# Performance work log

Measured on AMD Instinct MI355X. Metric: run time of the kernel, lower is better.

## Reference

```python
import jax, jax.numpy as jnp
from jax import lax
import numpy as np
import math

V, D, N, L, KC, KL, B, S = 32000, 1024, 64, 4, 4, 4, 2, 1024
SCALE = 1.0 / math.sqrt(2 * L)   # base_layer.residual_scale
GAMMA = 0.01                     # lindblad_gamma
COND_TH = 100.0                  # condition_threshold
PHASE = np.complex64(np.exp(1j * 0.1))  # quaternionic escape rotation


def setup_inputs() -> dict:
    key = jax.random.key(0)
    ks = jax.random.split(key, 16)
    g = lambda k, shp, s=0.02: jax.random.normal(k, shp, jnp.float32) * s
    return {
        'token_ids': jax.random.randint(ks[0], (B, S), 0, V, dtype=jnp.int32),
        'emb_r': g(ks[1], (V, D)),
        'emb_i': g(ks[2], (V, D)),
        'W_in': g(ks[3], (L, D, 2 * D)),
        'conv_k': g(ks[4], (L, D, KC), 0.2),
        'A_log': jax.random.normal(ks[5], (L, D, N), jnp.float32) * 0.5,
        'dt_scale': g(ks[6], (L, D), 1.0),
        'dt_bias': jnp.full((L, D), -2.0, jnp.float32),
        'W_B': g(ks[7], (L, N, D)),
        'W_C': g(ks[8], (L, N, D)),
        'D_skip': g(ks[9], (L, D), 0.1),
        'W_out': g(ks[10], (L, D, D)),
        'L_ops': g(ks[11], (L, KL, D), 0.1),
        'norm_w': jnp.ones((D,), jnp.float32),
    }


def _dwconv(x, k):
    # causal depthwise conv; x [B,S,D] real, k [D,KC]
    xt = jnp.transpose(x, (0, 2, 1))  # [B,D,S]
    pad = k.shape[-1] - 1
    y = lax.conv_general_dilated(xt, k[:, None, :], (1,), [(pad, 0)],
                                 feature_group_count=k.shape[0])
    return jnp.transpose(y, (0, 2, 1))


def _csilu(x):
    # complex 'silu': x * sigmoid(|x|)
    return x * jax.nn.sigmoid(jnp.abs(x))


def _layer(x, Wi, ck, Alog, dts, dtb, WB, WC, Dk, Wo, Lops):
    residual = x
    xz = jnp.einsum('bsd,de->bse', x, Wi)          # complex [B,S,2D]
    x1, z = xz[..., :D], xz[..., D:]
    x1 = _dwconv(x1.real, ck) + 1j * _dwconv(x1.imag, ck)
    x1 = _csilu(x1)
    dt = jax.nn.softplus(x1.real * dts + dtb)      # [B,S,D] real
    A = -jnp.exp(Alog)                             # [D,N] real, stable
    Bc = jnp.einsum('bsd,nd->bsn', x1, WB)         # complex [B,S,N]
    Cc = jnp.einsum('bsd,nd->bsn', x1, WC)

    def step(h, inp):
        dt_t, x_t, B_t, C_t = inp                  # [B,D],[B,D],[B,N],[B,N]
        decay = jnp.exp(dt_t[..., None] * A)       # [B,D,N] real
        h = decay * h + (dt_t * x_t)[..., None] * B_t[:, None, :]
        y = jnp.einsum('bdn,bn->bd', h, C_t)
        return h, y

    h0 = jnp.zeros((x.shape[0], D, N), jnp.complex64)
    xs = (jnp.transpose(dt, (1, 0, 2)), jnp.transpose(x1, (1, 0, 2)),
          jnp.transpose(Bc, (1, 0, 2)), jnp.transpose(Cc, (1, 0, 2)))
    _, ys = lax.scan(step, h0, xs)                 # [S,B,D]
    y = jnp.transpose(ys, (1, 0, 2)) + Dk * x1
    y = y * _csilu(z)
    branch = jnp.einsum('bsd,de->bse', y, Wo)      # branch_out = (out-res)/scale

    # Lindblad dissipation: psi -> psi - gamma * sum_k L_k (L_k^H psi)
    proj = jnp.einsum('bsd,kd->bsk', branch, Lops)
    branch = branch - GAMMA * jnp.einsum('bsk,kd->bsd', proj, Lops)

    # H_eff = mean_s |psi_s><psi_s|; quaternionic escape uses its conditioning.
    # Only the diagonal is needed for the (diag-approx) condition number.
    diag = jnp.mean(jnp.abs(branch) ** 2, axis=1)  # [B,D]
    cond = jnp.max(diag, -1) / (jnp.min(diag, -1) + 1e-8)
    phase = jnp.where(cond > COND_TH, PHASE, jnp.complex64(1.0))  # [B]
    branch = branch * phase[:, None, None]

    # hybrid automata: _H_prev is None on first forward -> no jump (faithful)
    return residual + SCALE * branch


def reference(token_ids, emb_r, emb_i, W_in, conv_k, A_log, dt_scale, dt_bias,
              W_B, W_C, D_skip, W_out, L_ops, norm_w):
    psi = emb_r[token_ids] + 1j * emb_i[token_ids]   # [B,S,D] complex64
    for l in range(L):
        psi = _layer(psi, W_in[l], conv_k[l], A_log[l], dt_scale[l],
                     dt_bias[l], W_B[l], W_C[l], D_skip[l], W_out[l], L_ops[l])
    # ComplexRMSNorm
    rms = jnp.sqrt(jnp.mean(jnp.abs(psi) ** 2, -1, keepdims=True) + 1e-8)
    psi = psi / rms * norm_w
    # Born collapse sampler with weight tied to real embedding
    amp_r = jnp.einsum('bsd,vd->bsv', psi.real, emb_r)
    amp_i = jnp.einsum('bsd,vd->bsv', psi.imag, emb_r)
    logits = jnp.log(amp_r ** 2 + amp_i ** 2 + 1e-8)  # [B,S,V] real
    return logits
```

## Files before the change

kernel.cpp:

```cpp
#include <hip/hip_runtime.h>
#include <math.h>

#define BB 2
#define SS 1024
#define DD 1024
#define NN 64
#define LLAYERS 4
#define KCC 4
#define KLL 4
#define VV 32000
#define MM (BB*SS)
#define M2 (2*MM)
#define PS ((size_t)MM*DD)
#define CH 4
#define LC (SS/CH)
#define BDW (BB*DD)

#define SCALE_F 0.35355339059327373f
#define GAMMA_F 0.01f
#define PHASE_COS 0.99500416527802576f
#define PHASE_SIN 0.09983341664682815f

typedef _Float16 f16x8 __attribute__((ext_vector_type(8)));
typedef _Float16 f16x4 __attribute__((ext_vector_type(4)));
typedef float f32x4 __attribute__((ext_vector_type(4)));

__device__ __forceinline__ float softplus_f(float x) {
    return fmaxf(x, 0.f) + log1pf(expf(-fabsf(x)));
}

__device__ __forceinline__ void async16(void* lds_dst, const void* g_src) {
    __builtin_amdgcn_global_load_lds(
        (const __attribute__((address_space(1))) unsigned int*)g_src,
        (__attribute__((address_space(3))) unsigned int*)lds_dst,
        16, 0, 0);
}

__device__ __forceinline__ float rsum64_dpp(float v) {
    int x;
    x = __float_as_int(v);
    v += __int_as_float(__builtin_amdgcn_update_dpp(0, x, 0x111, 0xf, 0xf, true));
    x = __float_as_int(v);
    v += __int_as_float(__builtin_amdgcn_update_dpp(0, x, 0x112, 0xf, 0xf, true));
    x = __float_as_int(v);
    v += __int_as_float(__builtin_amdgcn_update_dpp(0, x, 0x114, 0xf, 0xf, true));
    x = __float_as_int(v);
    v += __int_as_float(__builtin_amdgcn_update_dpp(0, x, 0x118, 0xf, 0xf, true));
    x = __float_as_int(v);
    v += __int_as_float(__builtin_amdgcn_update_dpp(0, x, 0x142, 0xa, 0xf, true));
    x = __float_as_int(v);
    v += __int_as_float(__builtin_amdgcn_update_dpp(0, x, 0x143, 0xc, 0xf, true));
    return v;
}

__global__ __launch_bounds__(256) void k_split_w(const float* __restrict__ W,
        _Float16* __restrict__ Wh, _Float16* __restrict__ Wl, int Ksz, int Nsz) {
    __shared__ float t[32][33];
    int k0 = blockIdx.x * 32, n0 = blockIdx.y * 32;
    size_t base = (size_t)blockIdx.z * Ksz * Nsz;
    int r = threadIdx.x >> 3, c4 = (threadIdx.x & 7) * 4;
    float4 v = *(const float4*)(W + base + (size_t)(k0 + r) * Nsz + n0 + c4);
    t[r][c4 + 0] = v.x; t[r][c4 + 1] = v.y; t[r][c4 + 2] = v.z; t[r][c4 + 3] = v.w;
    __syncthreads();
    f16x4 hi, lo;
    #pragma unroll
    for (int j = 0; j < 4; ++j) {
        float x = t[c4 + j][r];
        _Float16 h = (_Float16)x;
        hi[j] = h; lo[j] = (_Float16)(x - (float)h);
    }
    size_t o = base + (size_t)(n0 + r) * Ksz + k0 + c4;
    *(f16x4*)(Wh + o) = hi;
    *(f16x4*)(Wl + o) = lo;
}

__global__ __launch_bounds__(256) void k_embed(const int* __restrict__ tok,
        const float* __restrict__ er, const float* __restrict__ ei,
        float* __restrict__ Pr, float* __restrict__ Pi,
        _Float16* __restrict__ Ph, _Float16* __restrict__ Pl) {
    int i = blockIdx.x * 256 + threadIdx.x;
    int d4 = (i & (DD/4 - 1)) * 4;
    int m  = i >> 8;
    int t = tok[m];
    float4 r  = *(const float4*)(er + (size_t)t * DD + d4);
    float4 im = *(const float4*)(ei + (size_t)t * DD + d4);
    size_t o = (size_t)m * DD + d4;
    *(float4*)(Pr + o) = r;
    *(float4*)(Pi + o) = im;
    float vr[4] = {r.x, r.y, r.z, r.w}, vi[4] = {im.x, im.y, im.z, im.w};
    f16x4 rh, rl, ih, il;
    #pragma unroll
    for (int j = 0; j < 4; ++j) {
        _Float16 h = (_Float16)vr[j]; rh[j] = h; rl[j] = (_Float16)(vr[j] - (float)h);
        _Float16 g = (_Float16)vi[j]; ih[j] = g; il[j] = (_Float16)(vi[j] - (float)g);
    }
    *(f16x4*)(Ph + o) = rh;      *(f16x4*)(Pl + o) = rl;
    *(f16x4*)(Ph + PS + o) = ih; *(f16x4*)(Pl + PS + o) = il;
}

__global__ __launch_bounds__(256, 2) void k_gemm_f16(
        const _Float16* __restrict__ Ah, const _Float16* __restrict__ Al,
        const _Float16* __restrict__ Bh, const _Float16* __restrict__ Bl,
        float* __restrict__ C, int Nsz) {
    __shared__ __align__(16) unsigned char lds[32768];
    const int lane = threadIdx.x & 63;
    const int wid  = threadIdx.x >> 6;
    const int wm = (wid >> 1) * 64;
    const int wv = (wid & 1) * 64;
    const int n0 = blockIdx.x * 128;
    const int m0 = blockIdx.y * 128;
    const int fr = lane & 15, fq = lane >> 4;

    f32x4 acc[4][4] = {};

    for (int k0 = 0; k0 < 1024; k0 += 32) {
        #pragma unroll
        for (int j = 0; j < 8; ++j) {
            int cid = wid * 8 + j;
            int sel = cid >> 3, c = cid & 7;
            const _Float16* bp = (sel == 0) ? Ah : (sel == 1) ? Al : (sel == 2) ? Bh : Bl;
            int rbase = ((sel < 2) ? m0 : n0) + c * 16 + fr;
            async16(lds + cid * 1024, bp + (size_t)rbase * 1024 + k0 + fq * 8);
        }
        __syncthreads();

        f16x8 ah[4], al[4];
        #pragma unroll
        for (int ms = 0; ms < 4; ++ms) {
            int off = ((wm >> 4) + ms) * 1024 + lane * 16;
            ah[ms] = *(const f16x8*)(lds + off);
            al[ms] = *(const f16x8*)(lds + 8192 + off);
        }
        #pragma unroll
        for (int vs = 0; vs < 4; ++vs) {
            int boff = ((wv >> 4) + vs) * 1024 + lane * 16;
            f16x8 bh = *(const f16x8*)(lds + 16384 + boff);
            f16x8 bl = *(const f16x8*)(lds + 24576 + boff);
            #pragma unroll
            for (int ms = 0; ms < 4; ++ms) {
                acc[ms][vs] = __builtin_amdgcn_mfma_f32_16x16x32_f16(ah[ms], bh, acc[ms][vs], 0, 0, 0);
                acc[ms][vs] = __builtin_amdgcn_mfma_f32_16x16x32_f16(ah[ms], bl, acc[ms][vs], 0, 0, 0);
                acc[ms][vs] = __builtin_amdgcn_mfma_f32_16x16x32_f16(al[ms], bh, acc[ms][vs], 0, 0, 0);
            }
        }
        __syncthreads();
    }

    #pragma unroll
    for (int ms = 0; ms < 4; ++ms) {
        #pragma unroll
        for (int vs = 0; vs < 4; ++vs) {
            #pragma unroll
            for (int r = 0; r < 4; ++r) {
                int row = m0 + wm + ms * 16 + fq * 4 + r;
                int col = n0 + wv + vs * 16 + fr;
                C[(size_t)row * Nsz + col] = acc[ms][vs][r];
            }
        }
    }
}

__global__ __launch_bounds__(256) void k_conv(const float* __restrict__ XZ,
        const float* __restrict__ ck, const float* __restrict__ dts,
        const float* __restrict__ dtb,
        float* __restrict__ Xr, float* __restrict__ Xi, float* __restrict__ DT,
        float* __restrict__ ZUr, float* __restrict__ ZUi) {
    int i = blockIdx.x * 256 + threadIdx.x;
    int d = i & (DD - 1);
    int m = i >> 10;
    int b = m >> 10, s = m & (SS - 1);
    float cr = 0.f, ci = 0.f;
    #pragma unroll
    for (int j = 0; j < KCC; ++j) {
        int sj = s - (KCC - 1) + j;
        if (sj >= 0) {
            int mm = (b << 10) + sj;
            float kw = ck[d * KCC + j];
            cr = fmaf(XZ[(size_t)mm * 2048 + d], kw, cr);
            ci = fmaf(XZ[(size_t)(MM + mm) * 2048 + d], kw, ci);
        }
    }
    float mag = sqrtf(cr*cr + ci*ci);
    float sg = 1.f / (1.f + expf(-mag));
    float xr = cr * sg, xi = ci * sg;
    Xr[i] = xr; Xi[i] = xi;
    DT[i] = softplus_f(fmaf(xr, dts[d], dtb[d]));
    float zr = XZ[(size_t)m * 2048 + DD + d];
    float zi = XZ[(size_t)(MM + m) * 2048 + DD + d];
    float mz = sqrtf(zr*zr + zi*zi);
    float sz = 1.f / (1.f + expf(-mz));
    ZUr[i] = zr * sz; ZUi[i] = zi * sz;
}

__global__ __launch_bounds__(256) void k_bc(const float* __restrict__ X,
        const float* __restrict__ WBp, const float* __restrict__ WCp,
        float* __restrict__ BC2) {
    __shared__ float xs[4][DD];
    __shared__ float red[4 * 256];
    int r0 = blockIdx.x * 4;
    for (int f = threadIdx.x; f < 4 * (DD / 4); f += 256) {
        int r = f / (DD / 4), c = (f % (DD / 4)) * 4;
        *(float4*)(&xs[r][c]) = *(const float4*)(X + (size_t)(r0 + r) * DD + c);
    }
    __syncthreads();
    int out = threadIdx.x & 127;
    int half = threadIdx.x >> 7;
    const float* Wrow = (out < 64) ? (WBp + (size_t)out * DD) : (WCp + (size_t)(out - 64) * DD);
    float acc[4] = {0.f, 0.f, 0.f, 0.f};
    for (int k = half * 512; k < half * 512 + 512; k += 4) {
        float4 w = *(const float4*)(Wrow + k);
        #pragma unroll
        for (int r = 0; r < 4; ++r) {
            float4 x4 = *(float4*)(&xs[r][k]);
            acc[r] = fmaf(x4.x, w.x, fmaf(x4.y, w.y, fmaf(x4.z, w.z, fmaf(x4.w, w.w, acc[r]))));
        }
    }
    #pragma unroll
    for (int r = 0; r < 4; ++r) red[r * 256 + threadIdx.x] = acc[r];
    __syncthreads();
    if (threadIdx.x < 128) {
        int isIm = (r0 >= MM) ? 1 : 0;
        int n = out & 63;
        int comp = ((out >> 6) << 1) | isIm;
        #pragma unroll
        for (int r = 0; r < 4; ++r) {
            float v = red[r * 256 + threadIdx.x] + red[r * 256 + threadIdx.x + 128];
            int m = (r0 + r) & (MM - 1);
            BC2[((size_t)m * 64 + n) * 4 + comp] = v;
        }
    }
}

__global__ __launch_bounds__(256, 8) void k_scan1(const float* __restrict__ X,
        const float* __restrict__ DT, const float4* __restrict__ BC2,
        const float* __restrict__ Alog, float* __restrict__ Y2T,
        float2* __restrict__ HB, float* __restrict__ SDT) {
    int w = (blockIdx.x << 2) + (threadIdx.x >> 6);
    int lane = threadIdx.x & 63;
    int c = w & (CH - 1);
    int bd = w >> 2;
    int b = bd >> 10, d = bd & (DD - 1);
    float Av = -__expf(Alog[(size_t)d * NN + lane]);
    float hr = 0.f, hi = 0.f, sdt = 0.f;
    int s0 = c * LC, s1 = s0 + LC;
    size_t mBase = (size_t)(b << 10);
    size_t md = (mBase + s0) * DD + d;
    float dt_c = DT[md], xr_c = X[md], xi_c = X[PS + md];
    float4 bc_c = BC2[(mBase + s0) * 64 + lane];
    size_t ys = (size_t)bd * SS + s0;
    for (int s = s0; s < s1; ++s) {
        int sn = (s + 1 < s1) ? (s + 1) : s;
        size_t mdn = (mBase + sn) * DD + d;
        float dt_n = DT[mdn], xr_n = X[mdn], xi_n = X[PS + mdn];
        float4 bc_n = BC2[(mBase + sn) * 64 + lane];
        float g = __expf(dt_c * Av);
        float dxr = dt_c * xr_c, dxi = dt_c * xi_c;
        hr = fmaf(g, hr, fmaf(dxr, bc_c.x, -dxi * bc_c.y));
        hi = fmaf(g, hi, fmaf(dxr, bc_c.y,  dxi * bc_c.x));
        sdt += dt_c;
        float yr = rsum64_dpp(hr * bc_c.z - hi * bc_c.w);
        float yi = rsum64_dpp(hr * bc_c.w + hi * bc_c.z);
        if (lane == 63) {
            Y2T[ys]      = yr;
            Y2T[PS + ys] = yi;
        }
        ++ys;
        dt_c = dt_n; xr_c = xr_n; xi_c = xi_n; bc_c = bc_n;
    }
    HB[((size_t)c * BDW + bd) * NN + lane] = make_float2(hr, hi);
    if (lane == 0) SDT[c * BDW + bd] = sdt;
}

__global__ __launch_bounds__(256, 8) void k_scan3(const float* __restrict__ DT,
        const float* __restrict__ BC2, const float* __restrict__ Alog,
        const float2* __restrict__ HB, const float* __restrict__ SDT,
        float* __restrict__ Y2T) {
    int w = (blockIdx.x << 2) + (threadIdx.x >> 6);
    int lane = threadIdx.x & 63;
    int cm1 = w >> 11;
    int bd = w & (BDW - 1);
    int b = bd >> 10, d = bd & (DD - 1);
    float Av = -__expf(Alog[(size_t)d * NN + lane]);
    float2 h0 = HB[(size_t)bd * NN + lane];
    float hr = h0.x, hi = h0.y;
    if (cm1 >= 1) {
        float2 h1 = HB[((size_t)1 * BDW + bd) * NN + lane];
        float P1 = __expf(Av * SDT[1 * BDW + bd]);
        hr = fmaf(P1, hr, h1.x); hi = fmaf(P1, hi, h1.y);
        if (cm1 >= 2) {
            float2 h2 = HB[((size_t)2 * BDW + bd) * NN + lane];
            float P2 = __expf(Av * SDT[2 * BDW + bd]);
            hr = fmaf(P2, hr, h2.x); hi = fmaf(P2, hi, h2.y);
        }
    }
    int s0 = (cm1 + 1) * LC, s1 = s0 + LC;
    size_t mBase = (size_t)(b << 10);
    size_t md = (mBase + s0) * DD + d;
    float dt_c = DT[md];
    float2 cc_c = *(const float2*)(BC2 + ((mBase + s0) * 64 + lane) * 4 + 2);
    size_t ys = (size_t)bd * SS + s0;
    for (int s = s0; s < s1; ++s) {
        int sn = (s + 1 < s1) ? (s + 1) : s;
        size_t mdn = (mBase + sn) * DD + d;
        float dt_n = DT[mdn];
        float2 cc_n = *(const float2*)(BC2 + ((mBase + sn) * 64 + lane) * 4 + 2);
        float g = __expf(dt_c * Av);
        hr *= g; hi *= g;
        float yr = rsum64_dpp(hr * cc_c.x - hi * cc_c.y);
        float yi = rsum64_dpp(hr * cc_c.y + hi * cc_c.x);
        if (lane == 63) {
            Y2T[ys]      += yr;
            Y2T[PS + ys] += yi;
        }
        ++ys;
        dt_c = dt_n; cc_c = cc_n;
    }
}

__global__ __launch_bounds__(256) void k_ymod(const float* __restrict__ Y2T,
        const float* __restrict__ X, const float* __restrict__ ZUr,
        const float* __restrict__ ZUi, const float* __restrict__ Dk,
        _Float16* __restrict__ YOh, _Float16* __restrict__ YOl) {
    __shared__ float tr[64][65];
    __shared__ float ti[64][65];
    int d0 = blockIdx.x * 64, m0 = blockIdx.y * 64;
    int b = m0 >> 10, s0 = m0 & (SS - 1);
    int t = threadIdx.x;
    int rr = t >> 2, c0 = (t & 3) * 4;
    size_t ybase = (size_t)(b * DD + d0 + rr) * SS + s0;
    #pragma unroll
    for (int j = 0; j < 4; ++j) {
        float4 vr = *(const float4*)(Y2T + ybase + c0 + j * 16);
        float4 vi = *(const float4*)(Y2T + PS + ybase + c0 + j * 16);
        int sl = c0 + j * 16;
        tr[sl + 0][rr] = vr.x; tr[sl + 1][rr] = vr.y; tr[sl + 2][rr] = vr.z; tr[sl + 3][rr] = vr.w;
        ti[sl + 0][rr] = vi.x; ti[sl + 1][rr] = vi.y; ti[sl + 2][rr] = vi.z; ti[sl + 3][rr] = vi.w;
    }
    __syncthreads();
    int td = t & 63, tq = t >> 6;
    float dk = Dk[d0 + td];
    #pragma unroll
    for (int k = 0; k < 16; ++k) {
        int tm = tq * 16 + k;
        size_t i = (size_t)(m0 + tm) * DD + d0 + td;
        float yr = tr[tm][td];
        float yi = ti[tm][td];
        yr = fmaf(dk, X[i], yr);
        yi = fmaf(dk, X[PS + i], yi);
        float zr = ZUr[i], zi = ZUi[i];
        float or_ = yr * zr - yi * zi;
        float oi_ = yr * zi + yi * zr;
        _Float16 h0 = (_Float16)or_, h1 = (_Float16)oi_;
        YOh[i] = h0;      YOl[i] = (_Float16)(or_ - (float)h0);
        YOh[PS + i] = h1; YOl[PS + i] = (_Float16)(oi_ - (float)h1);
    }
}

__global__ __launch_bounds__(256) void k_projcorr(float* __restrict__ BR,
        const float* __restrict__ Lop) {
    int row = (blockIdx.x << 2) + (threadIdx.x >> 6);
    int lane = threadIdx.x & 63;
    float* br = BR + (size_t)row * DD;
    float4 v[4], lw[4][4];
    float acc[4] = {0.f, 0.f, 0.f, 0.f};
    #pragma unroll
    for (int j = 0; j < 4; ++j) {
        int col = lane * 4 + j * 256;
        v[j] = *(const float4*)(br + col);
        #pragma unroll
        for (int k = 0; k < 4; ++k) {
            lw[j][k] = *(const float4*)(Lop + (size_t)k * DD + col);
            acc[k] += v[j].x * lw[j][k].x + v[j].y * lw[j][k].y
                    + v[j].z * lw[j][k].z + v[j].w * lw[j][k].w;
        }
    }
    #pragma unroll
    for (int off = 1; off <= 32; off <<= 1) {
        #pragma unroll
        for (int k = 0; k < 4; ++k) acc[k] += __shfl_xor(acc[k], off, 64);
    }
    #pragma unroll
    for (int j = 0; j < 4; ++j) {
        int col = lane * 4 + j * 256;
        float4 o;
        o.x = v[j].x - GAMMA_F * (acc[0]*lw[j][0].x + acc[1]*lw[j][1].x + acc[2]*lw[j][2].x + acc[3]*lw[j][3].x);
        o.y = v[j].y - GAMMA_F * (acc[0]*lw[j][0].y + acc[1]*lw[j][1].y + acc[2]*lw[j][2].y + acc[3]*lw[j][3].y);
        o.z = v[j].z - GAMMA_F * (acc[0]*lw[j][0].z + acc[1]*lw[j][1].z + acc[2]*lw[j][2].z + acc[3]*lw[j][3].z);
        o.w = v[j].w - GAMMA_F * (acc[0]*lw[j][0].w + acc[1]*lw[j][1].w + acc[2]*lw[j][2].w + acc[3]*lw[j][3].w);
        *(float4*)(br + col) = o;
    }
}

__global__ __launch_bounds__(256) void k_diag(const float* __restrict__ BR,
        float* __restrict__ DG) {
    __shared__ float red[4][64];
    int b = blockIdx.y, d0 = blockIdx.x * 64;
    int sg = threadIdx.x >> 6, ld = threadIdx.x & 63;
    float acc = 0.f;
    for (int s = sg; s < SS; s += 4) {
        size_t m = (size_t)(b * SS + s) * DD + d0 + ld;
        float r = BR[m], ii = BR[PS + m];
        acc = fmaf(r, r, fmaf(ii, ii, acc));
    }
    red[sg][ld] = acc;
    __syncthreads();
    if (threadIdx.x < 64) {
        float v = red[0][threadIdx.x] + red[1][threadIdx.x] + red[2][threadIdx.x] + red[3][threadIdx.x];
        DG[b * DD + d0 + threadIdx.x] = v * (1.f / SS);
    }
}

__global__ __launch_bounds__(256) void k_phase(const float* __restrict__ DG,
        float* __restrict__ PH) {
    __shared__ float mx[256], mn[256];
    int b = blockIdx.x;
    float vmax = -1e30f, vmin = 1e30f;
    for (int d = threadIdx.x; d < DD; d += 256) {
        float v = DG[b * DD + d];
        vmax = fmaxf(vmax, v); vmin = fminf(vmin, v);
    }
    mx[threadIdx.x] = vmax; mn[threadIdx.x] = vmin;
    __syncthreads();
    for (int st = 128; st >= 1; st >>= 1) {
        if (threadIdx.x < st) {
            mx[threadIdx.x] = fmaxf(mx[threadIdx.x], mx[threadIdx.x + st]);
            mn[threadIdx.x] = fminf(mn[threadIdx.x], mn[threadIdx.x + st]);
        }
        __syncthreads();
    }
    if (threadIdx.x == 0) {
        float cond = mx[0] / (mn[0] + 1e-8f);
        bool ap = cond > 100.0f;
        PH[b * 2 + 0] = ap ? PHASE_COS : 1.f;
        PH[b * 2 + 1] = ap ? PHASE_SIN : 0.f;
    }
}

__global__ __launch_bounds__(256) void k_resid(float* __restrict__ Pr,
        float* __restrict__ Pi, const float* __restrict__ BR,
        const float* __restrict__ PH,
        _Float16* __restrict__ Ph, _Float16* __restrict__ Pl) {
    int i = blockIdx.x * 256 + threadIdx.x;
    int b = i >> 20;
    float pr = PH[b * 2], pih = PH[b * 2 + 1];
    float brr = BR[i], bri = BR[PS + i];
    float nr = fmaf(SCALE_F, brr * pr - bri * pih, Pr[i]);
    float ni = fmaf(SCALE_F, brr * pih + bri * pr, Pi[i]);
    Pr[i] = nr; Pi[i] = ni;
    _Float16 h0 = (_Float16)nr, h1 = (_Float16)ni;
    Ph[i] = h0;      Pl[i] = (_Float16)(nr - (float)h0);
    Ph[PS + i] = h1; Pl[PS + i] = (_Float16)(ni - (float)h1);
}

__global__ __launch_bounds__(256) void k_rms(const float* __restrict__ Pr,
        const float* __restrict__ Pi, const float* __restrict__ nw,
        _Float16* __restrict__ Sp) {
    __shared__ float red[256];
    int m = blockIdx.x;
    int d = threadIdx.x * 4;
    float4 r  = *(const float4*)(Pr + (size_t)m * DD + d);
    float4 ii = *(const float4*)(Pi + (size_t)m * DD + d);
    float acc = r.x*r.x + r.y*r.y + r.z*r.z + r.w*r.w
              + ii.x*ii.x + ii.y*ii.y + ii.z*ii.z + ii.w*ii.w;
    red[threadIdx.x] = acc;
    __syncthreads();
    for (int st = 128; st >= 1; st >>= 1) {
        if (threadIdx.x < st) red[threadIdx.x] += red[threadIdx.x + st];
        __syncthreads();
    }
    float inv = 1.f / sqrtf(red[0] * (1.f / DD) + 1e-8f);
    float4 w = *(const float4*)(nw + d);
    float qr[4] = {r.x*inv*w.x, r.y*inv*w.y, r.z*inv*w.z, r.w*inv*w.w};
    float qi[4] = {ii.x*inv*w.x, ii.y*inv*w.y, ii.z*inv*w.z, ii.w*inv*w.w};
    f16x4 rh, rl, ih, il;
    #pragma unroll
    for (int j = 0; j < 4; ++j) {
        _Float16 h = (_Float16)qr[j]; rh[j] = h; rl[j] = (_Float16)(qr[j] - (float)h);
        _Float16 g = (_Float16)qi[j]; ih[j] = g; il[j] = (_Float16)(qi[j] - (float)g);
    }
    size_t o = (size_t)m * DD + d;
    *(f16x4*)(Sp + o)          = rh;
    *(f16x4*)(Sp + PS + o)     = rl;
    *(f16x4*)(Sp + 2 * PS + o) = ih;
    *(f16x4*)(Sp + 3 * PS + o) = il;
}

__global__ __launch_bounds__(256) void k_split_e(const float* __restrict__ E,
        _Float16* __restrict__ Eh, _Float16* __restrict__ El) {
    size_t i = (size_t)(blockIdx.x * 256 + threadIdx.x) * 8;
    float4 a = *(const float4*)(E + i);
    float4 b = *(const float4*)(E + i + 4);
    float v[8] = {a.x, a.y, a.z, a.w, b.x, b.y, b.z, b.w};
    f16x8 hi, lo;
    #pragma unroll
    for (int j = 0; j < 8; ++j) {
        _Float16 h = (_Float16)v[j];
        hi[j] = h; lo[j] = (_Float16)(v[j] - (float)h);
    }
    *(f16x8*)(Eh + i) = hi;
    *(f16x8*)(El + i) = lo;
}

__global__ __launch_bounds__(256, 2) void k_logits_mfma(
        const _Float16* __restrict__ Sp,
        const _Float16* __restrict__ Eh, const _Float16* __restrict__ El,
        float* __restrict__ out) {
    __shared__ __align__(16) unsigned char lds[49152];
    const int lane = threadIdx.x & 63;
    const int wid  = threadIdx.x >> 6;
    const int wm = (wid >> 1) * 64;
    const int wv = (wid & 1) * 64;
    const int fr = lane & 15, fq = lane >> 4;
    int x = blockIdx.x & 7;
    int j = blockIdx.x >> 3;
    const int m0 = ((x << 1) | (j & 1)) << 7;
    const int v0 = (j >> 1) << 7;

    f32x4 accR[4][4] = {};
    f32x4 accI[4][4] = {};

    for (int k0 = 0; k0 < DD; k0 += 32) {
        #pragma unroll
        for (int jj = 0; jj < 12; ++jj) {
            int cid = jj * 4 + wid;
            const _Float16* src;
            int ldsoff;
            if (cid < 32) {
                int p = cid >> 3, c = cid & 7;
                src = Sp + (size_t)p * PS + (size_t)(m0 + c * 16 + fr) * DD + k0 + fq * 8;
                ldsoff = p * 8192 + c * 1024;
            } else {
                int r = cid - 32;
                int q = r >> 3, c = r & 7;
                const _Float16* Ep = q ? El : Eh;
                src = Ep + (size_t)(v0 + c * 16 + fr) * DD + k0 + fq * 8;
                ldsoff = 32768 + q * 8192 + c * 1024;
            }
            async16(lds + ldsoff, src);
        }
        __syncthreads();

        f16x8 aRh[4], aRl[4], aIh[4], aIl[4];
        #pragma unroll
        for (int ms = 0; ms < 4; ++ms) {
            int off = ((wm >> 4) + ms) * 1024 + lane * 16;
            aRh[ms] = *(const f16x8*)(lds + off);
            aRl[ms] = *(const f16x8*)(lds + 8192 + off);
            aIh[ms] = *(const f16x8*)(lds + 16384 + off);
            aIl[ms] = *(const f16x8*)(lds + 24576 + off);
        }
        #pragma unroll
        for (int vs = 0; vs < 4; ++vs) {
            int boff = ((wv >> 4) + vs) * 1024 + lane * 16;
            f16x8 bh = *(const f16x8*)(lds + 32768 + boff);
            f16x8 bl = *(const f16x8*)(lds + 40960 + boff);
            #pragma unroll
            for (int ms = 0; ms < 4; ++ms) {
                accR[ms][vs] = __builtin_amdgcn_mfma_f32_16x16x32_f16(aRh[ms], bh, accR[ms][vs], 0, 0, 0);
                accR[ms][vs] = __builtin_amdgcn_mfma_f32_16x16x32_f16(aRh[ms], bl, accR[ms][vs], 0, 0, 0);
                accR[ms][vs] = __builtin_amdgcn_mfma_f32_16x16x32_f16(aRl[ms], bh, accR[ms][vs], 0, 0, 0);
                accI[ms][vs] = __builtin_amdgcn_mfma_f32_16x16x32_f16(aIh[ms], bh, accI[ms][vs], 0, 0, 0);
                accI[ms][vs] = __builtin_amdgcn_mfma_f32_16x16x32_f16(aIh[ms], bl, accI[ms][vs], 0, 0, 0);
                accI[ms][vs] = __builtin_amdgcn_mfma_f32_16x16x32_f16(aIl[ms], bh, accI[ms][vs], 0, 0, 0);
            }
        }
        __syncthreads();
    }

    #pragma unroll
    for (int ms = 0; ms < 4; ++ms) {
        #pragma unroll
        for (int vs = 0; vs < 4; ++vs) {
            #pragma unroll
            for (int r = 0; r < 4; ++r) {
                int row = m0 + wm + ms * 16 + fq * 4 + r;
                int col = v0 + wv + vs * 16 + fr;
                float ar = accR[ms][vs][r], ai = accI[ms][vs][r];
                out[(size_t)row * VV + col] = logf(fmaf(ar, ar, fmaf(ai, ai, 1e-8f)));
            }
        }
    }
}

extern "C" void kernel_launch(void* const* d_in, const int* in_sizes, int n_in,
                              void* d_out, int out_size, void* d_ws, size_t ws_size,
                              hipStream_t stream) {
    const int*   tok  = (const int*)d_in[0];
    const float* er   = (const float*)d_in[1];
    const float* ei   = (const float*)d_in[2];
    const float* Win  = (const float*)d_in[3];
    const float* ck   = (const float*)d_in[4];
    const float* Alog = (const float*)d_in[5];
    const float* dts  = (const float*)d_in[6];
    const float* dtb  = (const float*)d_in[7];
    const float* WB   = (const float*)d_in[8];
    const float* WC   = (const float*)d_in[9];
    const float* Dk   = (const float*)d_in[10];
    const float* Wo   = (const float*)d_in[11];
    const float* Lop  = (const float*)d_in[12];
    const float* nw   = (const float*)d_in[13];
    float* out = (float*)d_out;

    float* W0   = (float*)d_ws;
    float* P    = W0;
    float* XZ   = W0 + 2 * PS;
    float* X    = W0 + 6 * PS;
    float* DTp  = W0 + 8 * PS;
    float* ZU   = W0 + 9 * PS;
    float* Y2T  = W0 + 11 * PS;
    _Float16* YOh = (_Float16*)(W0 + 19 * PS);
    _Float16* YOl = (_Float16*)(W0 + 20 * PS);
    _Float16* Ph  = (_Float16*)(W0 + 21 * PS);
    _Float16* Pl  = (_Float16*)(W0 + 22 * PS);
    float* BR   = XZ;
    float* BC2  = W0 + 23 * PS;
    float* DIAG = BC2 + (size_t)MM * 64 * 4;
    float* PH   = DIAG + BB * DD;
    float2* HB  = (float2*)(PH + 16);
    float* SDT  = (float*)(HB + (size_t)CH * BDW * NN);
    _Float16* Winh = (_Float16*)(W0 + 25 * PS);
    _Float16* Winl = (_Float16*)(W0 + 27 * PS);
    _Float16* Woh  = (_Float16*)(W0 + 29 * PS);
    _Float16* Wol  = (_Float16*)(W0 + 30 * PS);
    _Float16* Sp  = (_Float16*)(W0 + 2 * PS);
    _Float16* Ehp = (_Float16*)(W0 + 4 * PS);
    _Float16* Elp = (_Float16*)(W0 + 13 * PS);

    k_split_w<<<dim3(32, 64, 4), 256, 0, stream>>>(Win, Winh, Winl, 1024, 2048);
    k_split_w<<<dim3(32, 32, 4), 256, 0, stream>>>(Wo, Woh, Wol, 1024, 1024);

    k_embed<<<(int)(PS / 4 / 256), 256, 0, stream>>>(tok, er, ei, P, P + PS, Ph, Pl);

    for (int l = 0; l < LLAYERS; ++l) {
        const float* Lopl = Lop + (size_t)l * KLL * DD;
        const float* Alogl = Alog + (size_t)l * DD * NN;
        const _Float16* Wih = Winh + (size_t)l * 2048 * 1024;
        const _Float16* Wil = Winl + (size_t)l * 2048 * 1024;
        const _Float16* Wohl = Woh + (size_t)l * 1024 * 1024;
        const _Float16* Woll = Wol + (size_t)l * 1024 * 1024;

        k_gemm_f16<<<dim3(2048 / 128, M2 / 128), 256, 0, stream>>>(Ph, Pl, Wih, Wil, XZ, 2048);
        k_conv<<<(int)(MM * (size_t)DD / 256), 256, 0, stream>>>(XZ, ck + (size_t)l * DD * KCC,
                dts + l * DD, dtb + l * DD, X, X + PS, DTp, ZU, ZU + PS);
        k_bc<<<M2 / 4, 256, 0, stream>>>(X, WB + (size_t)l * NN * DD, WC + (size_t)l * NN * DD, BC2);
        k_scan1<<<(BDW * CH) / 4, 256, 0, stream>>>(X, DTp, (const float4*)BC2, Alogl, Y2T, HB, SDT);
        k_scan3<<<(BDW * 3) / 4, 256, 0, stream>>>(DTp, BC2, Alogl, HB, SDT, Y2T);
        k_ymod<<<dim3(DD / 64, MM / 64), 256, 0, stream>>>(Y2T, X, ZU, ZU + PS, Dk + l * DD, YOh, YOl);
        k_gemm_f16<<<dim3(1024 / 128, M2 / 128), 256, 0, stream>>>(YOh, YOl, Wohl, Woll, BR, 1024);
        k_projcorr<<<M2 / 4, 256, 0, stream>>>(BR, Lopl);
        k_diag<<<dim3(DD / 64, BB), 256, 0, stream>>>(BR, DIAG);
        k_phase<<<BB, 256, 0, stream>>>(DIAG, PH);
        k_resid<<<(int)(PS / 256), 256, 0, stream>>>(P, P + PS, BR, PH, Ph, Pl);
    }

    k_rms<<<MM, 256, 0, stream>>>(P, P + PS, nw, Sp);
    k_split_e<<<(int)((size_t)VV * DD / 8 / 256), 256, 0, stream>>>(er, Ehp, Elp);
    k_logits_mfma<<<4000, 256, 0, stream>>>(Sp, Ehp, Elp, out);
}
```

Measured before the change: 3.636 ms.

## Vectorize conv and residual kernels, add N64 GEMM tile, nontemporal logits stores

k_conv and k_resid now process four elements per thread with float4 and f16x4 loads and stores, which cuts instruction count and widens memory transactions. The output-projection GEMM switches to a new 128x64-tile kernel, giving twice as many blocks for N=1024 and better CU occupancy. The logits kernel writes its large output with nontemporal stores to avoid polluting the cache. These are several independent bandwidth and occupancy tweaks, and the main risk is that the new GEMM has lower per-block reuse.

Result: no change. 3.594 ms (-1.2%).

```diff
diff --git a/kernel.cpp b/kernel.cpp
--- a/kernel.cpp
+++ b/kernel.cpp
@@ -160,36 +160,136 @@
     }
 }
 
+__global__ __launch_bounds__(256, 2) void k_gemm_n64(
+        const _Float16* __restrict__ Ah, const _Float16* __restrict__ Al,
+        const _Float16* __restrict__ Bh, const _Float16* __restrict__ Bl,
+        float* __restrict__ C, int Nsz) {
+    __shared__ __align__(16) unsigned char lds[24576];
+    const int lane = threadIdx.x & 63;
+    const int wid  = threadIdx.x >> 6;
+    const int wm = (wid >> 1) * 64;
+    const int wv = (wid & 1) * 32;
+    const int n0 = blockIdx.x * 64;
+    const int m0 = blockIdx.y * 128;
+    const int fr = lane & 15, fq = lane >> 4;
+
+    f32x4 acc[4][2] = {};
+
+    for (int k0 = 0; k0 < 1024; k0 += 32) {
+        #pragma unroll
+        for (int j = 0; j < 6; ++j) {
+            int cid = j * 4 + wid;
+            const _Float16* bp;
+            int rbase, ldsoff;
+            if (cid < 16) {
+                bp = (cid >> 3) ? Al : Ah;
+                rbase = m0 + (cid & 7) * 16 + fr;
+                ldsoff = cid * 1024;
+            } else {
+                int r = cid - 16;
+                bp = (r >> 2) ? Bl : Bh;
+                rbase = n0 + (r & 3) * 16 + fr;
+                ldsoff = 16384 + r * 1024;
+            }
+            async16(lds + ldsoff, bp + (size_t)rbase * 1024 + k0 + fq * 8);
+        }
+        __syncthreads();
+
+        f16x8 ah[4], al[4];
+        #pragma unroll
+        for (int ms = 0; ms < 4; ++ms) {
+            int off = ((wm >> 4) + ms) * 1024 + lane * 16;
+            ah[ms] = *(const f16x8*)(lds + off);
+            al[ms] = *(const f16x8*)(lds + 8192 + off);
+        }
+        #pragma unroll
+        for (int vs = 0; vs < 2; ++vs) {
+            int boff = ((wv >> 4) + vs) * 1024 + lane * 16;
+            f16x8 bh = *(const f16x8*)(lds + 16384 + boff);
+            f16x8 bl = *(const f16x8*)(lds + 20480 + boff);
+            #pragma unroll
+            for (int ms = 0; ms < 4; ++ms) {
+                acc[ms][vs] = __builtin_amdgcn_mfma_f32_16x16x32_f16(ah[ms], bh, acc[ms][vs], 0, 0, 0);
+                acc[ms][vs] = __builtin_amdgcn_mfma_f32_16x16x32_f16(ah[ms], bl, acc[ms][vs], 0, 0, 0);
+                acc[ms][vs] = __builtin_amdgcn_mfma_f32_16x16x32_f16(al[ms], bh, acc[ms][vs], 0, 0, 0);
+            }
+        }
+        __syncthreads();
+    }
+
+    #pragma unroll
+    for (int ms = 0; ms < 4; ++ms) {
+        #pragma unroll
+        for (int vs = 0; vs < 2; ++vs) {
+            #pragma unroll
+            for (int r = 0; r < 4; ++r) {
+                int row = m0 + wm + ms * 16 + fq * 4 + r;
+                int col = n0 + wv + vs * 16 + fr;
+                C[(size_t)row * Nsz + col] = acc[ms][vs][r];
+            }
+        }
+    }
+}
+
 __global__ __launch_bounds__(256) void k_conv(const float* __restrict__ XZ,
         const float* __restrict__ ck, const float* __restrict__ dts,
         const float* __restrict__ dtb,
         float* __restrict__ Xr, float* __restrict__ Xi, float* __restrict__ DT,
         float* __restrict__ ZUr, float* __restrict__ ZUi) {
-    int i = blockIdx.x * 256 + threadIdx.x;
-    int d = i & (DD - 1);
-    int m = i >> 10;
+    int i4 = blockIdx.x * 256 + threadIdx.x;
+    int dq = (i4 & (DD / 4 - 1)) * 4;
+    int m  = i4 >> 8;
     int b = m >> 10, s = m & (SS - 1);
-    float cr = 0.f, ci = 0.f;
+    size_t i = (size_t)m * DD + dq;
+    float kw[4][4];
+    #pragma unroll
+    for (int c = 0; c < 4; ++c)
+        *(float4*)kw[c] = *(const float4*)(ck + (size_t)(dq + c) * KCC);
+    float cr[4] = {0.f, 0.f, 0.f, 0.f}, ci[4] = {0.f, 0.f, 0.f, 0.f};
     #pragma unroll
     for (int j = 0; j < KCC; ++j) {
         int sj = s - (KCC - 1) + j;
         if (sj >= 0) {
-            int mm = (b << 10) + sj;
-            float kw = ck[d * KCC + j];
-            cr = fmaf(XZ[(size_t)mm * 2048 + d], kw, cr);
-            ci = fmaf(XZ[(size_t)(MM + mm) * 2048 + d], kw, ci);
-        }
-    }
-    float mag = sqrtf(cr*cr + ci*ci);
-    float sg = 1.f / (1.f + expf(-mag));
-    float xr = cr * sg, xi = ci * sg;
-    Xr[i] = xr; Xi[i] = xi;
-    DT[i] = softplus_f(fmaf(xr, dts[d], dtb[d]));
-    float zr = XZ[(size_t)m * 2048 + DD + d];
-    float zi = XZ[(size_t)(MM + m) * 2048 + DD + d];
-    float mz = sqrtf(zr*zr + zi*zi);
-    float sz = 1.f / (1.f + expf(-mz));
-    ZUr[i] = zr * sz; ZUi[i] = zi * sz;
+            size_t mm = ((size_t)(b << 10) + sj) * 2048 + dq;
+            float4 xr4 = *(const float4*)(XZ + mm);
+            float4 xi4 = *(const float4*)(XZ + (size_t)MM * 2048 + mm);
+            float xr_[4] = {xr4.x, xr4.y, xr4.z, xr4.w};
+            float xi_[4] = {xi4.x, xi4.y, xi4.z, xi4.w};
+            #pragma unroll
+            for (int c = 0; c < 4; ++c) {
+                cr[c] = fmaf(xr_[c], kw[c][j], cr[c]);
+                ci[c] = fmaf(xi_[c], kw[c][j], ci[c]);
+            }
+        }
+    }
+    float4 dts4 = *(const float4*)(dts + dq);
+    float4 dtb4 = *(const float4*)(dtb + dq);
+    float dts_[4] = {dts4.x, dts4.y, dts4.z, dts4.w};
+    float dtb_[4] = {dtb4.x, dtb4.y, dtb4.z, dtb4.w};
+    float xro[4], xio[4], dto[4];
+    #pragma unroll
+    for (int c = 0; c < 4; ++c) {
+        float mag = sqrtf(cr[c] * cr[c] + ci[c] * ci[c]);
+        float sg = 1.f / (1.f + expf(-mag));
+        xro[c] = cr[c] * sg; xio[c] = ci[c] * sg;
+        dto[c] = softplus_f(fmaf(xro[c], dts_[c], dtb_[c]));
+    }
+    *(float4*)(Xr + i) = make_float4(xro[0], xro[1], xro[2], xro[3]);
+    *(float4*)(Xi + i) = make_float4(xio[0], xio[1], xio[2], xio[3]);
+    *(float4*)(DT + i) = make_float4(dto[0], dto[1], dto[2], dto[3]);
+    float4 zr4 = *(const float4*)(XZ + (size_t)m * 2048 + DD + dq);
+    float4 zi4 = *(const float4*)(XZ + (size_t)(MM + m) * 2048 + DD + dq);
+    float zr_[4] = {zr4.x, zr4.y, zr4.z, zr4.w};
+    float zi_[4] = {zi4.x, zi4.y, zi4.z, zi4.w};
+    float zur[4], zui[4];
+    #pragma unroll
+    for (int c = 0; c < 4; ++c) {
+        float mz = sqrtf(zr_[c] * zr_[c] + zi_[c] * zi_[c]);
+        float sz = 1.f / (1.f + expf(-mz));
+        zur[c] = zr_[c] * sz; zui[c] = zi_[c] * sz;
+    }
+    *(float4*)(ZUr + i) = make_float4(zur[0], zur[1], zur[2], zur[3]);
+    *(float4*)(ZUi + i) = make_float4(zui[0], zui[1], zui[2], zui[3]);
 }
 
 __global__ __launch_bounds__(256) void k_bc(const float* __restrict__ X,
@@ -440,16 +540,30 @@
         float* __restrict__ Pi, const float* __restrict__ BR,
         const float* __restrict__ PH,
         _Float16* __restrict__ Ph, _Float16* __restrict__ Pl) {
-    int i = blockIdx.x * 256 + threadIdx.x;
-    int b = i >> 20;
+    size_t i = ((size_t)blockIdx.x * 256 + threadIdx.x) * 4;
+    int b = (int)(i >> 20);
     float pr = PH[b * 2], pih = PH[b * 2 + 1];
-    float brr = BR[i], bri = BR[PS + i];
-    float nr = fmaf(SCALE_F, brr * pr - bri * pih, Pr[i]);
-    float ni = fmaf(SCALE_F, brr * pih + bri * pr, Pi[i]);
-    Pr[i] = nr; Pi[i] = ni;
-    _Float16 h0 = (_Float16)nr, h1 = (_Float16)ni;
-    Ph[i] = h0;      Pl[i] = (_Float16)(nr - (float)h0);
-    Ph[PS + i] = h1; Pl[PS + i] = (_Float16)(ni - (float)h1);
+    float4 brr4 = *(const float4*)(BR + i);
+    float4 bri4 = *(const float4*)(BR + PS + i);
+    float4 pr4  = *(const float4*)(Pr + i);
+    float4 pi4  = *(const float4*)(Pi + i);
+    float brr[4] = {brr4.x, brr4.y, brr4.z, brr4.w};
+    float bri[4] = {bri4.x, bri4.y, bri4.z, bri4.w};
+    float pro[4] = {pr4.x, pr4.y, pr4.z, pr4.w};
+    float pio[4] = {pi4.x, pi4.y, pi4.z, pi4.w};
+    f16x4 rh, rl, ih, il;
+    float nr[4], ni[4];
+    #pragma unroll
+    for (int c = 0; c < 4; ++c) {
+        nr[c] = fmaf(SCALE_F, brr[c] * pr - bri[c] * pih, pro[c]);
+        ni[c] = fmaf(SCALE_F, brr[c] * pih + bri[c] * pr, pio[c]);
+        _Float16 h0 = (_Float16)nr[c]; rh[c] = h0; rl[c] = (_Float16)(nr[c] - (float)h0);
+        _Float16 h1 = (_Float16)ni[c]; ih[c] = h1; il[c] = (_Float16)(ni[c] - (float)h1);
+    }
+    *(float4*)(Pr + i) = make_float4(nr[0], nr[1], nr[2], nr[3]);
+    *(float4*)(Pi + i) = make_float4(ni[0], ni[1], ni[2], ni[3]);
+    *(f16x4*)(Ph + i) = rh;      *(f16x4*)(Pl + i) = rl;
+    *(f16x4*)(Ph + PS + i) = ih; *(f16x4*)(Pl + PS + i) = il;
 }
 
 __global__ __launch_bounds__(256) void k_rms(const float* __restrict__ Pr,
@@ -576,7 +690,8 @@
                 int row = m0 + wm + ms * 16 + fq * 4 + r;
                 int col = v0 + wv + vs * 16 + fr;
                 float ar = accR[ms][vs][r], ai = accI[ms][vs][r];
-                out[(size_t)row * VV + col] = logf(fmaf(ar, ar, fmaf(ai, ai, 1e-8f)));
+                __builtin_nontemporal_store(logf(fmaf(ar, ar, fmaf(ai, ai, 1e-8f))),
+                                            out + (size_t)row * VV + col);
             }
         }
     }
@@ -640,17 +755,17 @@
         const _Float16* Woll = Wol + (size_t)l * 1024 * 1024;
 
         k_gemm_f16<<<dim3(2048 / 128, M2 / 128), 256, 0, stream>>>(Ph, Pl, Wih, Wil, XZ, 2048);
-        k_conv<<<(int)(MM * (size_t)DD / 256), 256, 0, stream>>>(XZ, ck + (size_t)l * DD * KCC,
+        k_conv<<<(int)(MM * (size_t)DD / 4 / 256), 256, 0, stream>>>(XZ, ck + (size_t)l * DD * KCC,
                 dts + l * DD, dtb + l * DD, X, X + PS, DTp, ZU, ZU + PS);
         k_bc<<<M2 / 4, 256, 0, stream>>>(X, WB + (size_t)l * NN * DD, WC + (size_t)l * NN * DD, BC2);
         k_scan1<<<(BDW * CH) / 4, 256, 0, stream>>>(X, DTp, (const float4*)BC2, Alogl, Y2T, HB, SDT);
         k_scan3<<<(BDW * 3) / 4, 256, 0, stream>>>(DTp, BC2, Alogl, HB, SDT, Y2T);
         k_ymod<<<dim3(DD / 64, MM / 64), 256, 0, stream>>>(Y2T, X, ZU, ZU + PS, Dk + l * DD, YOh, YOl);
-        k_gemm_f16<<<dim3(1024 / 128, M2 / 128), 256, 0, stream>>>(YOh, YOl, Wohl, Woll, BR, 1024);
+        k_gemm_n64<<<dim3(1024 / 64, M2 / 128), 256, 0, stream>>>(YOh, YOl, Wohl, Woll, BR, 1024);
         k_projcorr<<<M2 / 4, 256, 0, stream>>>(BR, Lopl);
         k_diag<<<dim3(DD / 64, BB), 256, 0, stream>>>(BR, DIAG);
         k_phase<<<BB, 256, 0, stream>>>(DIAG, PH);
-        k_resid<<<(int)(PS / 256), 256, 0, stream>>>(P, P + PS, BR, PH, Ph, Pl);
+        k_resid<<<(int)(PS / 4 / 256), 256, 0, stream>>>(P, P + PS, BR, PH, Ph, Pl);
     }
 
     k_rms<<<MM, 256, 0, stream>>>(P, P + PS, nw, Sp);
```
